# Optimization experiments

Hardware: AMD Instinct MI355X
Metric: run time of the kernel (lower is better)

The kernel has to match this reference:

```python
import jax, jax.numpy as jnp
import numpy as np

NUM_HEADS = 16
EMBED_DIM = 1024
HEAD_DIM = EMBED_DIM // NUM_HEADS


def setup_inputs() -> dict:
    key = jax.random.key(0)
    ks = jax.random.split(key, 9)
    B, S, D = 4, 2048, EMBED_DIM
    scale = 1.0 / np.sqrt(D)
    inp = {
        "x": jax.random.normal(ks[0], (B, S, D), dtype=jnp.float32),
        "Wq": jax.random.normal(ks[1], (D, D), dtype=jnp.float32) * scale,
        "bq": jnp.zeros((D,), dtype=jnp.float32),
        "Wk": jax.random.normal(ks[2], (D, D), dtype=jnp.float32) * scale,
        "bk": jnp.zeros((D,), dtype=jnp.float32),
        "Wv": jax.random.normal(ks[3], (D, D), dtype=jnp.float32) * scale,
        "bv": jnp.zeros((D,), dtype=jnp.float32),
        "Wo": jax.random.normal(ks[4], (D, D), dtype=jnp.float32) * scale,
        "bo": jnp.zeros((D,), dtype=jnp.float32),
    }
    return inp


def reference(x, Wq, bq, Wk, bk, Wv, bv, Wo, bo):
    # x: [B, S, D]; weights stored torch-style as [out, in] -> use x @ W.T + b
    B, S, D = x.shape
    H, Hd = NUM_HEADS, HEAD_DIM

    def proj(W, b):
        return (jnp.einsum('bsd,ed->bse', x, W) + b).reshape(B, S, H, Hd).transpose(0, 2, 1, 3)

    Q = proj(Wq, bq)  # [B, H, S, Hd]
    K = proj(Wk, bk)
    V = proj(Wv, bv)

    scores = jnp.einsum('bhqd,bhkd->bhqk', Q, K) / jnp.sqrt(jnp.float32(Hd))
    attn = jax.nn.softmax(scores, axis=-1)  # dropout is identity in eval mode
    context = jnp.einsum('bhqk,bhkd->bhqd', attn, V)
    context = context.transpose(0, 2, 1, 3).reshape(B, S, D)
    out = jnp.einsum('bsd,ed->bse', context, Wo) + bo
    return out
```

## Files before the change

### kernel.cpp

```cpp
#include <hip/hip_runtime.h>


#define LOG2E 1.4426950408889634f
#define QSCALE (0.125f * LOG2E)

typedef __bf16 bf16x8 __attribute__((ext_vector_type(8)));
typedef float f32x4 __attribute__((ext_vector_type(4)));
typedef float f32x2 __attribute__((ext_vector_type(2)));
typedef unsigned short u16x4 __attribute__((ext_vector_type(4)));
typedef unsigned short u16x8 __attribute__((ext_vector_type(8)));
typedef unsigned int u32x4 __attribute__((ext_vector_type(4)));

__device__ __forceinline__ unsigned short f2bf(float f) {
  unsigned int u = __builtin_bit_cast(unsigned int, f);
  u += 0x7fffu + ((u >> 16) & 1u);
  return (unsigned short)(u >> 16);
}

__device__ __forceinline__ unsigned int cvtpk(float a, float b) {
  unsigned int r;
  asm("v_cvt_pk_bf16_f32 %0, %1, %2" : "=v"(r) : "v"(a), "v"(b));
  return r;
}

typedef const __attribute__((address_space(1))) void* gptr_t;
typedef __attribute__((address_space(3))) void* lptr_t;
__device__ __forceinline__ void gload16(const void* g, void* l) {
  __builtin_amdgcn_global_load_lds((gptr_t)g, (lptr_t)l, 16, 0, 0);
}

__global__ __launch_bounds__(256) void k_cvt(const float* __restrict__ x,
                                             const float* __restrict__ Wq, const float* __restrict__ Wk,
                                             const float* __restrict__ Wv, const float* __restrict__ Wo,
                                             unsigned short* __restrict__ xb, unsigned short* __restrict__ Wb) {
  int gi = (blockIdx.x * 256 + threadIdx.x) * 4;
  if (gi < 8388608) {
    f32x4 v = *(const f32x4*)(x + gi);
    u16x4 o; o[0] = f2bf(v[0]); o[1] = f2bf(v[1]); o[2] = f2bf(v[2]); o[3] = f2bf(v[3]);
    *(u16x4*)(xb + gi) = o;
  } else {
    int i = gi - 8388608;
    int wsel = i >> 20;
    int loc = i & 1048575;
    const float* src = (wsel == 0) ? Wq : (wsel == 1) ? Wk : (wsel == 2) ? Wv : Wo;
    float sc = (wsel == 0) ? QSCALE : 1.0f;
    f32x4 v = *(const f32x4*)(src + loc);
    u16x4 o; o[0] = f2bf(v[0] * sc); o[1] = f2bf(v[1] * sc); o[2] = f2bf(v[2] * sc); o[3] = f2bf(v[3] * sc);
    *(u16x4*)(Wb + i) = o;
  }
}

__global__ __launch_bounds__(256, 2) void k_gemm_qkv(
    const unsigned short* __restrict__ xb, const unsigned short* __restrict__ Wb,
    const float* __restrict__ bq, const float* __restrict__ bk, const float* __restrict__ bv,
    unsigned short* __restrict__ Qb, unsigned short* __restrict__ Kb, unsigned short* __restrict__ Vtb) {
  __shared__ unsigned short As[128 * 32];
  __shared__ unsigned short Bs[128 * 32];
  const int tid = threadIdx.x;
  const int lane = tid & 63;
  const int w = tid >> 6;
  const int wm = w & 1;
  const int wn = w >> 1;
  const int lin = blockIdx.x + (blockIdx.y << 3) + (blockIdx.z << 9);
  const int swz = (lin & 7) * 192 + (lin >> 3);
  const int z = swz >> 9;
  const int m0 = ((swz >> 3) & 63) << 7;
  const int n0 = (swz & 7) << 7;
  const unsigned short* W = Wb + ((size_t)z << 20);

  const int srow = tid >> 2;
  const int sch = (tid & 3) << 3;
  const size_t a0 = (size_t)(m0 + srow) * 1024 + sch;
  const size_t b0 = (size_t)(n0 + srow) * 1024 + sch;

  f32x4 zero4 = {0.f, 0.f, 0.f, 0.f};
  f32x4 acc[4][4];
#pragma unroll
  for (int i = 0; i < 4; ++i)
#pragma unroll
    for (int jj = 0; jj < 4; ++jj) acc[i][jj] = zero4;

  const int fr = lane & 15;
  const int fk = (lane >> 4) << 3;

  for (int kt = 0; kt < 32; ++kt) {
    const int ko = kt << 5;
    __syncthreads();
    gload16(xb + a0 + ko, As + tid * 8);
    gload16(xb + a0 + (size_t)65536 + ko, As + 2048 + tid * 8);
    gload16(W + b0 + ko, Bs + tid * 8);
    gload16(W + b0 + (size_t)65536 + ko, Bs + 2048 + tid * 8);
    __syncthreads();
    bf16x8 af[4], bfr[4];
#pragma unroll
    for (int mt = 0; mt < 4; ++mt)
      af[mt] = *(const bf16x8*)&As[(wm * 64 + mt * 16 + fr) * 32 + fk];
#pragma unroll
    for (int nt = 0; nt < 4; ++nt)
      bfr[nt] = *(const bf16x8*)&Bs[(wn * 64 + nt * 16 + fr) * 32 + fk];
#pragma unroll
    for (int mt = 0; mt < 4; ++mt)
#pragma unroll
      for (int nt = 0; nt < 4; ++nt)
        acc[mt][nt] = __builtin_amdgcn_mfma_f32_16x16x32_bf16(af[mt], bfr[nt], acc[mt][nt], 0, 0, 0);
  }

  const float* bias = (z == 0) ? bq : (z == 1) ? bk : bv;
  const float bsc = (z == 0) ? QSCALE : 1.0f;
  const int rg = (lane >> 4) << 2;
#pragma unroll
  for (int mt = 0; mt < 4; ++mt) {
    const int mb = m0 + wm * 64 + mt * 16 + rg;
    const int b = mb >> 11;
    const int s = mb & 2047;
#pragma unroll
    for (int nt = 0; nt < 4; ++nt) {
      const int n = n0 + wn * 64 + nt * 16 + fr;
      const float bvv = bias[n] * bsc;
      const int h = n >> 6;
      const int d = n & 63;
      if (z == 2) {
        u16x4 pk;
#pragma unroll
        for (int r = 0; r < 4; ++r) pk[r] = f2bf(acc[mt][nt][r] + bvv);
        const int pbase = (s & ~31) | ((s & 12) << 1) | ((s & 16) >> 2);
        *(u16x4*)&Vtb[(((size_t)(b * 16 + h) << 6) + d) * 2048 + pbase] = pk;
      } else {
        unsigned short* O = (z == 0) ? Qb : Kb;
#pragma unroll
        for (int r = 0; r < 4; ++r)
          O[(((size_t)(b * 16 + h) << 11) + s + r) * 64 + d] = f2bf(acc[mt][nt][r] + bvv);
      }
    }
  }
}

__global__ __launch_bounds__(512, 4) void k_flash(
    const unsigned short* __restrict__ Qb, const unsigned short* __restrict__ Kb,
    const unsigned short* __restrict__ Vtb, unsigned short* __restrict__ Ctx) {
  __shared__ unsigned short Ks[2 * 128 * 64];
  __shared__ unsigned short Vts[64 * 128];
  const int tid = threadIdx.x;
  const int lane = tid & 63;
  const int wq = tid >> 6;
  const int fr = lane & 15;
  const int qd = lane >> 4;
  const int lin = blockIdx.x + (blockIdx.y << 3);
  const int swz = ((lin & 7) << 6) + (lin >> 3);
  const int bh = swz >> 3;
  const int q0 = (swz & 7) << 8;
  const size_t hoff = (size_t)bh << 17;
  const unsigned short* Qh = Qb + hoff + ((size_t)q0 << 6);

  const unsigned short* kg[2];
  const unsigned short* vg[2];
  unsigned short* kl[2];
  unsigned short* vl[2];
#pragma unroll
  for (int p = 0; p < 2; ++p) {
    int slot = p * 512 + tid;
    int kr = slot >> 3, ch = slot & 7;
    kg[p] = Kb + hoff + (size_t)kr * 64 + ((ch ^ (kr & 7)) << 3);
    kl[p] = Ks + slot * 8;
    int dr = slot >> 4, ch2 = slot & 15;
    vg[p] = Vtb + hoff + (size_t)dr * 2048 + ((ch2 ^ (dr & 15)) << 3);
    vl[p] = Vts + slot * 8;
  }

  int kbase[2];
#pragma unroll
  for (int ds = 0; ds < 2; ++ds)
    kbase[ds] = fr * 64 + (((ds * 4 + qd) ^ (fr & 7)) << 3);
  int vbase[4];
#pragma unroll
  for (int ks = 0; ks < 4; ++ks)
    vbase[ks] = fr * 128 + (((ks * 4 + qd) ^ fr) << 3);

  bf16x8 qf[2][2];
#pragma unroll
  for (int qt = 0; qt < 2; ++qt)
#pragma unroll
    for (int ds = 0; ds < 2; ++ds)
      qf[qt][ds] = *(const bf16x8*)&Qh[(wq * 32 + qt * 16 + fr) * 64 + ds * 32 + qd * 8];

  f32x4 zero4 = {0.f, 0.f, 0.f, 0.f};
  f32x4 o_acc[2][4];
  f32x2 l2[2] = {{0.f, 0.f}, {0.f, 0.f}};
#pragma unroll
  for (int mt = 0; mt < 2; ++mt)
#pragma unroll
    for (int dt = 0; dt < 4; ++dt) o_acc[mt][dt] = zero4;

#pragma unroll
  for (int p = 0; p < 2; ++p) gload16(kg[p], kl[p]);
#pragma unroll
  for (int p = 0; p < 2; ++p) kg[p] += 128 * 64;
  __syncthreads();

  int curoff = 0;
  for (int j = 0; j < 16; ++j) {
#pragma unroll
    for (int p = 0; p < 2; ++p) gload16(vg[p], vl[p]);
#pragma unroll
    for (int p = 0; p < 2; ++p) gload16(kg[p], kl[p] + (curoff ^ 8192));
#pragma unroll
    for (int p = 0; p < 2; ++p) { kg[p] += 128 * 64; vg[p] += 128; }

    const unsigned short* Kc = Ks + curoff;
    u32x4 pfw[2][4];
#pragma unroll
    for (int ks = 0; ks < 4; ++ks) {
      f32x4 st0[2], st1[2];
      st0[0] = zero4; st0[1] = zero4; st1[0] = zero4; st1[1] = zero4;
      __builtin_amdgcn_s_setprio(1);
#pragma unroll
      for (int ds = 0; ds < 2; ++ds) {
        bf16x8 kf0 = *(const bf16x8*)&Kc[kbase[ds] + (2 * ks) * 1024];
        bf16x8 kf1 = *(const bf16x8*)&Kc[kbase[ds] + (2 * ks + 1) * 1024];
        st0[0] = __builtin_amdgcn_mfma_f32_16x16x32_bf16(kf0, qf[0][ds], st0[0], 0, 0, 0);
        st0[1] = __builtin_amdgcn_mfma_f32_16x16x32_bf16(kf0, qf[1][ds], st0[1], 0, 0, 0);
        st1[0] = __builtin_amdgcn_mfma_f32_16x16x32_bf16(kf1, qf[0][ds], st1[0], 0, 0, 0);
        st1[1] = __builtin_amdgcn_mfma_f32_16x16x32_bf16(kf1, qf[1][ds], st1[1], 0, 0, 0);
      }
      __builtin_amdgcn_s_setprio(0);
#pragma unroll
      for (int mt = 0; mt < 2; ++mt) {
#pragma unroll
        for (int r = 0; r < 4; ++r) {
          st0[mt][r] = __builtin_amdgcn_exp2f(st0[mt][r]);
          st1[mt][r] = __builtin_amdgcn_exp2f(st1[mt][r]);
        }
        f32x2 s01 = {st0[mt][0], st0[mt][1]};
        f32x2 s23 = {st0[mt][2], st0[mt][3]};
        f32x2 t01 = {st1[mt][0], st1[mt][1]};
        f32x2 t23 = {st1[mt][2], st1[mt][3]};
        l2[mt] += (s01 + s23) + (t01 + t23);
        u32x4 pk;
        pk[0] = cvtpk(st0[mt][0], st0[mt][1]);
        pk[1] = cvtpk(st0[mt][2], st0[mt][3]);
        pk[2] = cvtpk(st1[mt][0], st1[mt][1]);
        pk[3] = cvtpk(st1[mt][2], st1[mt][3]);
        pfw[mt][ks] = pk;
      }
    }

    asm volatile("s_waitcnt vmcnt(2)" ::: "memory");
    __builtin_amdgcn_s_barrier();

    __builtin_amdgcn_s_setprio(1);
#pragma unroll
    for (int ks = 0; ks < 4; ++ks) {
      bf16x8 pf0 = __builtin_bit_cast(bf16x8, pfw[0][ks]);
      bf16x8 pf1 = __builtin_bit_cast(bf16x8, pfw[1][ks]);
#pragma unroll
      for (int dt = 0; dt < 4; ++dt) {
        bf16x8 vf = *(const bf16x8*)&Vts[vbase[ks] + dt * 2048];
        o_acc[0][dt] = __builtin_amdgcn_mfma_f32_16x16x32_bf16(pf0, vf, o_acc[0][dt], 0, 0, 0);
        o_acc[1][dt] = __builtin_amdgcn_mfma_f32_16x16x32_bf16(pf1, vf, o_acc[1][dt], 0, 0, 0);
      }
    }
    __builtin_amdgcn_s_setprio(0);

    asm volatile("s_waitcnt vmcnt(0)" ::: "memory");
    __builtin_amdgcn_s_barrier();
    curoff ^= 8192;
  }

  float l_red[2];
#pragma unroll
  for (int mt = 0; mt < 2; ++mt) {
    float lv = l2[mt][0] + l2[mt][1];
    lv += __shfl_xor(lv, 16);
    lv += __shfl_xor(lv, 32);
    l_red[mt] = lv;
  }

  const int b = bh >> 4;
  const int h = bh & 15;
#pragma unroll
  for (int mt = 0; mt < 2; ++mt) {
#pragma unroll
    for (int r = 0; r < 4; ++r) {
      float lv = __shfl(l_red[mt], qd * 4 + r);
      float rl = 1.0f / lv;
      int s = q0 + wq * 32 + mt * 16 + qd * 4 + r;
      size_t base = (((size_t)b * 2048 + s) << 10) + (h << 6);
#pragma unroll
      for (int dt = 0; dt < 4; ++dt) Ctx[base + dt * 16 + fr] = f2bf(o_acc[mt][dt][r] * rl);
    }
  }
}

__global__ __launch_bounds__(256, 2) void k_gemm_out(
    const unsigned short* __restrict__ Ctx, const unsigned short* __restrict__ Wo,
    const float* __restrict__ bo, float* __restrict__ out) {
  __shared__ unsigned short As[128 * 32];
  __shared__ unsigned short Bs[128 * 32];
  const int tid = threadIdx.x;
  const int lane = tid & 63;
  const int w = tid >> 6;
  const int wm = w & 1;
  const int wn = w >> 1;
  const int lin = blockIdx.x + (blockIdx.y << 3);
  const int swz = ((lin & 7) << 6) + (lin >> 3);
  const int m0 = (swz >> 3) << 7;
  const int n0 = (swz & 7) << 7;

  const int srow = tid >> 2;
  const int sch = (tid & 3) << 3;
  const size_t a0 = (size_t)(m0 + srow) * 1024 + sch;
  const size_t b0 = (size_t)(n0 + srow) * 1024 + sch;

  f32x4 zero4 = {0.f, 0.f, 0.f, 0.f};
  f32x4 acc[4][4];
#pragma unroll
  for (int i = 0; i < 4; ++i)
#pragma unroll
    for (int jj = 0; jj < 4; ++jj) acc[i][jj] = zero4;

  const int fr = lane & 15;
  const int fk = (lane >> 4) << 3;

  for (int kt = 0; kt < 32; ++kt) {
    const int ko = kt << 5;
    __syncthreads();
    gload16(Ctx + a0 + ko, As + tid * 8);
    gload16(Ctx + a0 + (size_t)65536 + ko, As + 2048 + tid * 8);
    gload16(Wo + b0 + ko, Bs + tid * 8);
    gload16(Wo + b0 + (size_t)65536 + ko, Bs + 2048 + tid * 8);
    __syncthreads();
    bf16x8 af[4], bfr[4];
#pragma unroll
    for (int mt = 0; mt < 4; ++mt)
      af[mt] = *(const bf16x8*)&As[(wm * 64 + mt * 16 + fr) * 32 + fk];
#pragma unroll
    for (int nt = 0; nt < 4; ++nt)
      bfr[nt] = *(const bf16x8*)&Bs[(wn * 64 + nt * 16 + fr) * 32 + fk];
#pragma unroll
    for (int mt = 0; mt < 4; ++mt)
#pragma unroll
      for (int nt = 0; nt < 4; ++nt)
        acc[mt][nt] = __builtin_amdgcn_mfma_f32_16x16x32_bf16(af[mt], bfr[nt], acc[mt][nt], 0, 0, 0);
  }

  const int rg = (lane >> 4) << 2;
#pragma unroll
  for (int mt = 0; mt < 4; ++mt) {
    const int mb = m0 + wm * 64 + mt * 16 + rg;
#pragma unroll
    for (int nt = 0; nt < 4; ++nt) {
      const int n = n0 + wn * 64 + nt * 16 + fr;
      const float bvv = bo[n];
#pragma unroll
      for (int r = 0; r < 4; ++r)
        out[(size_t)(mb + r) * 1024 + n] = acc[mt][nt][r] + bvv;
    }
  }
}

extern "C" void kernel_launch(void* const* d_in, const int* in_sizes, int n_in,
                              void* d_out, int out_size, void* d_ws, size_t ws_size,
                              hipStream_t stream) {
  (void)in_sizes; (void)n_in; (void)out_size; (void)ws_size;
  const float* x = (const float*)d_in[0];
  const float* Wq = (const float*)d_in[1];
  const float* bq = (const float*)d_in[2];
  const float* Wk = (const float*)d_in[3];
  const float* bk = (const float*)d_in[4];
  const float* Wv = (const float*)d_in[5];
  const float* bv = (const float*)d_in[6];
  const float* Wo = (const float*)d_in[7];
  const float* bo = (const float*)d_in[8];
  float* out = (float*)d_out;

  unsigned short* xb = (unsigned short*)d_ws;
  unsigned short* Wb = xb + 8388608;
  unsigned short* Qb = Wb + 4194304;
  unsigned short* Kb = Qb + 8388608;
  unsigned short* Vtb = Kb + 8388608;
  unsigned short* Ctx = xb;

  k_cvt<<<12288, 256, 0, stream>>>(x, Wq, Wk, Wv, Wo, xb, Wb);
  k_gemm_qkv<<<dim3(8, 64, 3), 256, 0, stream>>>(xb, Wb, bq, bk, bv, Qb, Kb, Vtb);
  k_flash<<<dim3(8, 64), 512, 0, stream>>>(Qb, Kb, Vtb, Ctx);
  k_gemm_out<<<dim3(8, 64), 256, 0, stream>>>(Ctx, Wb + 3 * 1048576, bo, out);
}
```

Before: 263.9 us.

## Double-buffer LDS with XOR-swizzled layout in projection GEMMs

```diff
diff --git a/kernel.cpp b/kernel.cpp
--- a/kernel.cpp
+++ b/kernel.cpp
@@ -50,12 +50,12 @@
   }
 }
 
-__global__ __launch_bounds__(256, 2) void k_gemm_qkv(
+__global__ __launch_bounds__(256, 3) void k_gemm_qkv(
     const unsigned short* __restrict__ xb, const unsigned short* __restrict__ Wb,
     const float* __restrict__ bq, const float* __restrict__ bk, const float* __restrict__ bv,
     unsigned short* __restrict__ Qb, unsigned short* __restrict__ Kb, unsigned short* __restrict__ Vtb) {
-  __shared__ unsigned short As[128 * 32];
-  __shared__ unsigned short Bs[128 * 32];
+  __shared__ unsigned short As[2 * 4096];
+  __shared__ unsigned short Bs[2 * 4096];
   const int tid = threadIdx.x;
   const int lane = tid & 63;
   const int w = tid >> 6;
@@ -68,10 +68,25 @@
   const int n0 = (swz & 7) << 7;
   const unsigned short* W = Wb + ((size_t)z << 20);
 
-  const int srow = tid >> 2;
-  const int sch = (tid & 3) << 3;
-  const size_t a0 = (size_t)(m0 + srow) * 1024 + sch;
-  const size_t b0 = (size_t)(n0 + srow) * 1024 + sch;
+  const int sR = tid >> 3;
+  const int sc_ = (tid & 7) ^ (sR & 7);
+  const int mrow0 = 2 * sR + (sc_ >> 2);
+  const int kc0 = (sc_ & 3) << 3;
+  const unsigned short* srcA = xb + (size_t)(m0 + mrow0) * 1024 + kc0;
+  const unsigned short* srcB = W + (size_t)(n0 + mrow0) * 1024 + kc0;
+  unsigned short* dstA = As + tid * 8;
+  unsigned short* dstB = Bs + tid * 8;
+
+  const int fr = lane & 15;
+  const int kq = lane >> 4;
+  int aoff[4], boff[4];
+#pragma unroll
+  for (int t = 0; t < 4; ++t) {
+    int ra = wm * 64 + t * 16 + fr;
+    aoff[t] = ((ra >> 1) << 6) + (((((ra & 1) << 2) + kq) ^ ((ra >> 1) & 7)) << 3);
+    int rb = wn * 64 + t * 16 + fr;
+    boff[t] = ((rb >> 1) << 6) + (((((rb & 1) << 2) + kq) ^ ((rb >> 1) & 7)) << 3);
+  }
 
   f32x4 zero4 = {0.f, 0.f, 0.f, 0.f};
   f32x4 acc[4][4];
@@ -80,34 +95,47 @@
 #pragma unroll
     for (int jj = 0; jj < 4; ++jj) acc[i][jj] = zero4;
 
-  const int fr = lane & 15;
-  const int fk = (lane >> 4) << 3;
-
+  gload16(srcA, dstA);
+  gload16(srcA + 65536, dstA + 2048);
+  gload16(srcB, dstB);
+  gload16(srcB + 65536, dstB + 2048);
+
+  int cur = 0;
   for (int kt = 0; kt < 32; ++kt) {
-    const int ko = kt << 5;
-    __syncthreads();
-    gload16(xb + a0 + ko, As + tid * 8);
-    gload16(xb + a0 + (size_t)65536 + ko, As + 2048 + tid * 8);
-    gload16(W + b0 + ko, Bs + tid * 8);
-    gload16(W + b0 + (size_t)65536 + ko, Bs + 2048 + tid * 8);
-    __syncthreads();
+    const int kon = ((kt + 1) & 31) << 5;
+    const int soff = (cur ^ 1) << 12;
+    gload16(srcA + kon, dstA + soff);
+    gload16(srcA + 65536 + kon, dstA + soff + 2048);
+    gload16(srcB + kon, dstB + soff);
+    gload16(srcB + 65536 + kon, dstB + soff + 2048);
+
+    asm volatile("s_waitcnt vmcnt(4)" ::: "memory");
+    __builtin_amdgcn_s_barrier();
+
+    const unsigned short* Ac = As + (cur << 12);
+    const unsigned short* Bc = Bs + (cur << 12);
     bf16x8 af[4], bfr[4];
 #pragma unroll
-    for (int mt = 0; mt < 4; ++mt)
-      af[mt] = *(const bf16x8*)&As[(wm * 64 + mt * 16 + fr) * 32 + fk];
-#pragma unroll
-    for (int nt = 0; nt < 4; ++nt)
-      bfr[nt] = *(const bf16x8*)&Bs[(wn * 64 + nt * 16 + fr) * 32 + fk];
+    for (int mt = 0; mt < 4; ++mt) af[mt] = *(const bf16x8*)&Ac[aoff[mt]];
+#pragma unroll
+    for (int nt = 0; nt < 4; ++nt) bfr[nt] = *(const bf16x8*)&Bc[boff[nt]];
+
+    asm volatile("s_waitcnt lgkmcnt(0)" ::: "memory");
+    __builtin_amdgcn_s_barrier();
+
+    __builtin_amdgcn_s_setprio(1);
 #pragma unroll
     for (int mt = 0; mt < 4; ++mt)
 #pragma unroll
       for (int nt = 0; nt < 4; ++nt)
         acc[mt][nt] = __builtin_amdgcn_mfma_f32_16x16x32_bf16(af[mt], bfr[nt], acc[mt][nt], 0, 0, 0);
+    __builtin_amdgcn_s_setprio(0);
+    cur ^= 1;
   }
 
   const float* bias = (z == 0) ? bq : (z == 1) ? bk : bv;
   const float bsc = (z == 0) ? QSCALE : 1.0f;
-  const int rg = (lane >> 4) << 2;
+  const int rg = kq << 2;
 #pragma unroll
   for (int mt = 0; mt < 4; ++mt) {
     const int mb = m0 + wm * 64 + mt * 16 + rg;
@@ -291,11 +319,11 @@
   }
 }
 
-__global__ __launch_bounds__(256, 2) void k_gemm_out(
+__global__ __launch_bounds__(256, 3) void k_gemm_out(
     const unsigned short* __restrict__ Ctx, const unsigned short* __restrict__ Wo,
     const float* __restrict__ bo, float* __restrict__ out) {
-  __shared__ unsigned short As[128 * 32];
-  __shared__ unsigned short Bs[128 * 32];
+  __shared__ unsigned short As[2 * 4096];
+  __shared__ unsigned short Bs[2 * 4096];
   const int tid = threadIdx.x;
   const int lane = tid & 63;
   const int w = tid >> 6;
@@ -306,10 +334,25 @@
   const int m0 = (swz >> 3) << 7;
   const int n0 = (swz & 7) << 7;
 
-  const int srow = tid >> 2;
-  const int sch = (tid & 3) << 3;
-  const size_t a0 = (size_t)(m0 + srow) * 1024 + sch;
-  const size_t b0 = (size_t)(n0 + srow) * 1024 + sch;
+  const int sR = tid >> 3;
+  const int sc_ = (tid & 7) ^ (sR & 7);
+  const int mrow0 = 2 * sR + (sc_ >> 2);
+  const int kc0 = (sc_ & 3) << 3;
+  const unsigned short* srcA = Ctx + (size_t)(m0 + mrow0) * 1024 + kc0;
+  const unsigned short* srcB = Wo + (size_t)(n0 + mrow0) * 1024 + kc0;
+  unsigned short* dstA = As + tid * 8;
+  unsigned short* dstB = Bs + tid * 8;
+
+  const int fr = lane & 15;
+  const int kq = lane >> 4;
+  int aoff[4], boff[4];
+#pragma unroll
+  for (int t = 0; t < 4; ++t) {
+    int ra = wm * 64 + t * 16 + fr;
+    aoff[t] = ((ra >> 1) << 6) + (((((ra & 1) << 2) + kq) ^ ((ra >> 1) & 7)) << 3);
+    int rb = wn * 64 + t * 16 + fr;
+    boff[t] = ((rb >> 1) << 6) + (((((rb & 1) << 2) + kq) ^ ((rb >> 1) & 7)) << 3);
+  }
 
   f32x4 zero4 = {0.f, 0.f, 0.f, 0.f};
   f32x4 acc[4][4];
@@ -318,32 +361,45 @@
 #pragma unroll
     for (int jj = 0; jj < 4; ++jj) acc[i][jj] = zero4;
 
-  const int fr = lane & 15;
-  const int fk = (lane >> 4) << 3;
-
+  gload16(srcA, dstA);
+  gload16(srcA + 65536, dstA + 2048);
+  gload16(srcB, dstB);
+  gload16(srcB + 65536, dstB + 2048);
+
+  int cur = 0;
   for (int kt = 0; kt < 32; ++kt) {
-    const int ko = kt << 5;
-    __syncthreads();
-    gload16(Ctx + a0 + ko, As + tid * 8);
-    gload16(Ctx + a0 + (size_t)65536 + ko, As + 2048 + tid * 8);
-    gload16(Wo + b0 + ko, Bs + tid * 8);
-    gload16(Wo + b0 + (size_t)65536 + ko, Bs + 2048 + tid * 8);
-    __syncthreads();
+    const int kon = ((kt + 1) & 31) << 5;
+    const int soff = (cur ^ 1) << 12;
+    gload16(srcA + kon, dstA + soff);
+    gload16(srcA + 65536 + kon, dstA + soff + 2048);
+    gload16(srcB + kon, dstB + soff);
+    gload16(srcB + 65536 + kon, dstB + soff + 2048);
+
+    asm volatile("s_waitcnt vmcnt(4)" ::: "memory");
+    __builtin_amdgcn_s_barrier();
+
+    const unsigned short* Ac = As + (cur << 12);
+    const unsigned short* Bc = Bs + (cur << 12);
     bf16x8 af[4], bfr[4];
 #pragma unroll
-    for (int mt = 0; mt < 4; ++mt)
-      af[mt] = *(const bf16x8*)&As[(wm * 64 + mt * 16 + fr) * 32 + fk];
-#pragma unroll
-    for (int nt = 0; nt < 4; ++nt)
-      bfr[nt] = *(const bf16x8*)&Bs[(wn * 64 + nt * 16 + fr) * 32 + fk];
+    for (int mt = 0; mt < 4; ++mt) af[mt] = *(const bf16x8*)&Ac[aoff[mt]];
+#pragma unroll
+    for (int nt = 0; nt < 4; ++nt) bfr[nt] = *(const bf16x8*)&Bc[boff[nt]];
+
+    asm volatile("s_waitcnt lgkmcnt(0)" ::: "memory");
+    __builtin_amdgcn_s_barrier();
+
+    __builtin_amdgcn_s_setprio(1);
 #pragma unroll
     for (int mt = 0; mt < 4; ++mt)
 #pragma unroll
       for (int nt = 0; nt < 4; ++nt)
         acc[mt][nt] = __builtin_amdgcn_mfma_f32_16x16x32_bf16(af[mt], bfr[nt], acc[mt][nt], 0, 0, 0);
-  }
-
-  const int rg = (lane >> 4) << 2;
+    __builtin_amdgcn_s_setprio(0);
+    cur ^= 1;
+  }
+
+  const int rg = kq << 2;
 #pragma unroll
   for (int mt = 0; mt < 4; ++mt) {
     const int mb = m0 + wm * 64 + mt * 16 + rg;
```

Result: no change. 263.0 us (-0.3%).
